# Optimization experiments

Hardware: AMD Instinct MI355X
Metric: run time of the kernel (lower is better)

Reference implementation:

```python
import jax, jax.numpy as jnp
import numpy as np

N_NODES = 100000
N_EDGES = 3200000
IN_CH = 256


def setup_inputs() -> dict:
    key = jax.random.key(0)
    k1, k2, k3 = jax.random.split(key, 3)
    x = jax.random.normal(k1, (N_NODES, IN_CH), dtype=jnp.float32)
    edge_index = jax.random.randint(k2, (2, N_EDGES), 0, N_NODES, dtype=jnp.int64)
    # GCNConv linear: weight [in_channels, 1] (applied as x @ W), bias [1]
    W = jax.random.normal(k3, (IN_CH, 1), dtype=jnp.float32) * (1.0 / np.sqrt(IN_CH))
    b = jnp.zeros((1,), dtype=jnp.float32)
    return {"x": x, "edge_index": edge_index, "W": W, "b": b}


def reference(x, edge_index, W, b):
    # PyG GCNConv(in, 1): h = x @ W; add self-loops; symmetric norm; scatter-add to target; + bias
    N = x.shape[0]
    self_loops = jnp.broadcast_to(jnp.arange(N, dtype=edge_index.dtype)[None, :], (2, N))
    ei = jnp.concatenate([edge_index, self_loops], axis=1)  # [2, E+N]
    src, dst = ei[0], ei[1]

    # degree computed at target (col) with unit edge weights, incl. self-loops
    deg = jax.ops.segment_sum(jnp.ones(ei.shape[1], dtype=x.dtype), dst, num_segments=N)
    deg_inv_sqrt = jnp.where(deg > 0, jax.lax.rsqrt(deg), 0.0)
    norm = deg_inv_sqrt[src] * deg_inv_sqrt[dst]  # [E+N]

    h = x @ W  # [N, 1] — project first (out_channels < in_channels)
    msg = norm[:, None] * h[src]  # [E+N, 1]
    out = jax.ops.segment_sum(msg, dst, num_segments=N)  # [N, 1]
    return out + b
```

## Files before the change

kernel.cpp:

```cpp
#include <hip/hip_runtime.h>

#define GCN_N 100000
#define GCN_E 3200000
#define GCN_C 256

#define BSHIFT 8
#define NBUCK 391
#define BCAP 9216
#define NBP 512
#define NB4 1024
#define CHUNK (GCN_E / NB4)
#define TB 512
#define PERTHR ((CHUNK + TB - 1) / TB)

__global__ void __launch_bounds__(TB) k_proj_hist(const float* __restrict__ x,
                                                  const float* __restrict__ W,
                                                  float* __restrict__ h,
                                                  const int* __restrict__ dst,
                                                  int* __restrict__ cnts) {
    __shared__ int hist[NBUCK];
    const int tid = threadIdx.x;

    if (blockIdx.x < NBP) {
        const int lane   = tid & 63;
        const int wave   = (blockIdx.x * TB + tid) >> 6;
        const int nwaves = NBP * (TB / 64);
        const float4 wf = *reinterpret_cast<const float4*>(W + lane * 4);
        for (int i = wave * 4; i < GCN_N; i += nwaves * 4) {
            const float4 a0 = *reinterpret_cast<const float4*>(x + (size_t)(i + 0) * GCN_C + lane * 4);
            const float4 a1 = *reinterpret_cast<const float4*>(x + (size_t)(i + 1) * GCN_C + lane * 4);
            const float4 a2 = *reinterpret_cast<const float4*>(x + (size_t)(i + 2) * GCN_C + lane * 4);
            const float4 a3 = *reinterpret_cast<const float4*>(x + (size_t)(i + 3) * GCN_C + lane * 4);
            float s0 = a0.x * wf.x + a0.y * wf.y + a0.z * wf.z + a0.w * wf.w;
            float s1 = a1.x * wf.x + a1.y * wf.y + a1.z * wf.z + a1.w * wf.w;
            float s2 = a2.x * wf.x + a2.y * wf.y + a2.z * wf.z + a2.w * wf.w;
            float s3 = a3.x * wf.x + a3.y * wf.y + a3.z * wf.z + a3.w * wf.w;
            #pragma unroll
            for (int off = 32; off > 0; off >>= 1) {
                s0 += __shfl_down(s0, off, 64);
                s1 += __shfl_down(s1, off, 64);
                s2 += __shfl_down(s2, off, 64);
                s3 += __shfl_down(s3, off, 64);
            }
            if (lane == 0) {
                h[i + 0] = s0; h[i + 1] = s1; h[i + 2] = s2; h[i + 3] = s3;
            }
        }
        return;
    }

    const int blk = blockIdx.x - NBP;
    for (int b = tid; b < NBUCK; b += TB) hist[b] = 0;
    __syncthreads();
    const int c0 = blk * CHUNK;
    for (int k = tid; k < CHUNK; k += TB)
        atomicAdd(&hist[dst[c0 + k] >> BSHIFT], 1);
    __syncthreads();
    for (int b = tid; b < NBUCK; b += TB)
        cnts[(size_t)blk * NBUCK + b] = hist[b];
}

__global__ void __launch_bounds__(1024) k_scan(int* __restrict__ cb, int* __restrict__ fill) {
    __shared__ int wsum[16], woff[16];
    const int b = blockIdx.x, tid = threadIdx.x;
    const int lane = tid & 63, w = tid >> 6;
    const int v = cb[(size_t)tid * NBUCK + b];
    int incl = v;
    #pragma unroll
    for (int d = 1; d < 64; d <<= 1) {
        const int t = __shfl_up(incl, d, 64);
        if (lane >= d) incl += t;
    }
    if (lane == 63) wsum[w] = incl;
    __syncthreads();
    if (tid == 0) {
        int s = 0;
        #pragma unroll
        for (int k = 0; k < 16; ++k) { woff[k] = s; s += wsum[k]; }
    }
    __syncthreads();
    const int excl = incl - v + woff[w];
    cb[(size_t)tid * NBUCK + b] = b * BCAP + excl;
    if (tid == 1023) fill[b] = min(excl + v, BCAP);
}

__global__ void __launch_bounds__(TB) k_place(const int* __restrict__ src,
                                              const int* __restrict__ dst,
                                              const int* __restrict__ bases,
                                              int* __restrict__ bpack) {
    __shared__ int hist[NBUCK];
    __shared__ int lscan[NBUCK];
    __shared__ int base_s[NBUCK];
    __shared__ int wsum[8], woff[8];
    __shared__ int spack[CHUNK];
    __shared__ int sdest[CHUNK];
    const int tid = threadIdx.x, blk = blockIdx.x;

    for (int b = tid; b < NBUCK; b += TB) {
        hist[b]   = 0;
        base_s[b] = bases[(size_t)blk * NBUCK + b];
    }
    __syncthreads();

    const int c0 = blk * CHUNK;
    int my_off[PERTHR];
    #pragma unroll
    for (int j = 0; j < PERTHR; ++j) {
        const int k = tid + j * TB;
        if (k < CHUNK)
            my_off[j] = atomicAdd(&hist[dst[c0 + k] >> BSHIFT], 1);
    }
    __syncthreads();

    {
        int v = (tid < NBUCK) ? hist[tid] : 0;
        const int lane = tid & 63, w = tid >> 6;
        int incl = v;
        #pragma unroll
        for (int d = 1; d < 64; d <<= 1) {
            const int t = __shfl_up(incl, d, 64);
            if (lane >= d) incl += t;
        }
        if (lane == 63) wsum[w] = incl;
        __syncthreads();
        if (tid == 0) {
            int s = 0;
            #pragma unroll
            for (int k = 0; k < 8; ++k) { woff[k] = s; s += wsum[k]; }
        }
        __syncthreads();
        if (tid < NBUCK) lscan[tid] = incl - v + woff[w];
    }
    __syncthreads();

    #pragma unroll
    for (int j = 0; j < PERTHR; ++j) {
        const int k = tid + j * TB;
        if (k < CHUNK) {
            const int d = dst[c0 + k];
            const int s = src[c0 + k];
            const int b = d >> BSHIFT;
            const int off  = my_off[j];
            const int slot = lscan[b] + off;
            const int gpos = base_s[b] + off;
            spack[slot] = (s << BSHIFT) | (d & 255);
            sdest[slot] = (gpos < (b + 1) * BCAP) ? gpos : -1;
        }
    }
    __syncthreads();

    for (int i = tid; i < CHUNK; i += TB) {
        const int dpos = sdest[i];
        if (dpos >= 0) bpack[dpos] = spack[i];
    }
}

__global__ void __launch_bounds__(1024) k_deg_norm(const int* __restrict__ bpack,
                                                   const int* __restrict__ fill,
                                                   const float* __restrict__ h,
                                                   float* __restrict__ dis,
                                                   float* __restrict__ g) {
    __shared__ int cnt[256];
    const int p = blockIdx.x, tid = threadIdx.x;
    if (tid < 256) cnt[tid] = 0;
    __syncthreads();
    const int s0 = p * BCAP, s1 = s0 + fill[p];
    for (int i = s0 + tid; i < s1; i += 1024)
        atomicAdd(&cnt[bpack[i] & 255], 1);
    __syncthreads();
    if (tid < 256) {
        const int node = (p << BSHIFT) + tid;
        if (node < GCN_N) {
            const float r = rsqrtf(1.0f + (float)cnt[tid]);
            dis[node] = r;
            g[node]   = r * h[node];
        }
    }
}

__global__ void __launch_bounds__(1024) k_scatter_bin(const int* __restrict__ bpack,
                                                      const int* __restrict__ fill,
                                                      const float* __restrict__ g,
                                                      const float* __restrict__ dis,
                                                      const float* __restrict__ bias,
                                                      float* __restrict__ out) {
    __shared__ float acc[256];
    const int p = blockIdx.x, tid = threadIdx.x;
    if (tid < 256) acc[tid] = 0.0f;
    __syncthreads();
    const int s0 = p * BCAP, s1 = s0 + fill[p];
    for (int i = s0 + tid; i < s1; i += 1024) {
        const int pk = bpack[i];
        atomicAdd(&acc[pk & 255], g[pk >> BSHIFT]);
    }
    __syncthreads();
    if (tid < 256) {
        const int node = (p << BSHIFT) + tid;
        if (node < GCN_N)
            out[node] = bias[0] + dis[node] * (acc[tid] + g[node]);
    }
}


__global__ void k_zero(float* __restrict__ a, int n) {
    int i = blockIdx.x * blockDim.x + threadIdx.x;
    const int stride = gridDim.x * blockDim.x;
    for (; i < n; i += stride) a[i] = 0.0f;
}
__global__ void k_proj_sep(const float* __restrict__ x, const float* __restrict__ W,
                           float* __restrict__ h, int n) {
    const int lane   = threadIdx.x & 63;
    const int wave   = (blockIdx.x * blockDim.x + threadIdx.x) >> 6;
    const int nwaves = (gridDim.x * blockDim.x) >> 6;
    const float4 wf = *reinterpret_cast<const float4*>(W + lane * 4);
    for (int i = wave; i < n; i += nwaves) {
        const float4 xv = *reinterpret_cast<const float4*>(x + (size_t)i * GCN_C + lane * 4);
        float s = xv.x * wf.x + xv.y * wf.y + xv.z * wf.z + xv.w * wf.w;
        #pragma unroll
        for (int off = 32; off > 0; off >>= 1)
            s += __shfl_down(s, off, 64);
        if (lane == 0) h[i] = s;
    }
}
__global__ void k_degree_flat(const int* __restrict__ dst, float* __restrict__ deg, int e) {
    int i = blockIdx.x * blockDim.x + threadIdx.x;
    const int stride = gridDim.x * blockDim.x;
    for (; i < e; i += stride) atomicAdd(&deg[dst[i]], 1.0f);
}
__global__ void k_norm_flat(const float* __restrict__ h, float* __restrict__ deg_dis,
                            float* __restrict__ out, const float* __restrict__ bias, int n) {
    const int i = blockIdx.x * blockDim.x + threadIdx.x;
    if (i < n) {
        const float r = rsqrtf(deg_dis[i] + 1.0f);
        deg_dis[i] = r;
        out[i] = bias[0] + r * r * h[i];
    }
}
__global__ void k_scatter_flat(const int* __restrict__ src, const int* __restrict__ dst,
                               const float* __restrict__ h, const float* __restrict__ dis,
                               float* __restrict__ out, int e) {
    int i = blockIdx.x * blockDim.x + threadIdx.x;
    const int stride = gridDim.x * blockDim.x;
    for (; i < e; i += stride) {
        const int s = src[i], d = dst[i];
        atomicAdd(&out[d], dis[s] * dis[d] * h[s]);
    }
}

extern "C" void kernel_launch(void* const* d_in, const int* in_sizes, int n_in,
                              void* d_out, int out_size, void* d_ws, size_t ws_size,
                              hipStream_t stream) {
    const float* x  = (const float*)d_in[0];
    const int*   ei = (const int*)d_in[1];
    const float* W  = (const float*)d_in[2];
    const float* b  = (const float*)d_in[3];
    float* out = (float*)d_out;

    const int* src = ei;
    const int* dst = ei + GCN_E;

    const size_t need = ((size_t)3 * GCN_N + NBUCK
                         + (size_t)NB4 * NBUCK
                         + (size_t)NBUCK * BCAP) * 4;
    if (ws_size >= need) {
        float* h    = (float*)d_ws;
        float* dis  = h + GCN_N;
        float* g    = dis + GCN_N;
        int*   fill = (int*)(g + GCN_N);
        int*   cb   = fill + NBUCK;
        int*   bpack = cb + (size_t)NB4 * NBUCK;

        k_proj_hist<<<NBP + NB4, TB, 0, stream>>>(x, W, h, dst, cb);
        k_scan<<<NBUCK, 1024, 0, stream>>>(cb, fill);
        k_place<<<NB4, TB, 0, stream>>>(src, dst, cb, bpack);
        k_deg_norm<<<NBUCK, 1024, 0, stream>>>(bpack, fill, h, dis, g);
        k_scatter_bin<<<NBUCK, 1024, 0, stream>>>(bpack, fill, g, dis, b, out);
    } else {
        float* h   = (float*)d_ws;
        float* deg = h + GCN_N;
        k_zero<<<512, 256, 0, stream>>>(deg, GCN_N);
        k_proj_sep<<<2048, 256, 0, stream>>>(x, W, h, GCN_N);
        k_degree_flat<<<2048, 256, 0, stream>>>(dst, deg, GCN_E);
        k_norm_flat<<<(GCN_N + 255) / 256, 256, 0, stream>>>(h, deg, out, b, GCN_N);
        k_scatter_flat<<<2048, 256, 0, stream>>>(src, dst, h, deg, out, GCN_E);
    }
}
```

Baseline: 73.14 us.

## Fuse GCN pipeline into single cooperative kernel with grid syncs

Replaces the five-kernel bucketed GCN pipeline with one cooperative kernel of 512 blocks. Grid-wide syncs separate the projection and histogram, scan, placement, degree and scatter phases. Per-block state such as edge tags, local scan and the bucket contents stays in shared memory across phases, so edges are not re-read from global memory. Placement uses a binary search over the local scan instead of a separate destination array. This removes kernel launch gaps and redundant traffic, at the cost of four grid barriers, large LDS use that limits occupancy, and reliance on cooperative launch support.

Measured after the change: 73.33 us. About the same (+0.3%).

```diff
diff --git a/kernel.cpp b/kernel.cpp
--- a/kernel.cpp
+++ b/kernel.cpp
@@ -1,17 +1,190 @@
 #include <hip/hip_runtime.h>
+#include <hip/hip_cooperative_groups.h>
+
+namespace cg = cooperative_groups;
 
 #define GCN_N 100000
 #define GCN_E 3200000
 #define GCN_C 256
-
 #define BSHIFT 8
 #define NBUCK 391
 #define BCAP 9216
+
+#define NBLK 512
+#define TBM 1024
+#define CHUNKM (GCN_E / NBLK)
+#define PERTHRM ((CHUNKM + TBM - 1) / TBM)
+
 #define NBP 512
 #define NB4 1024
 #define CHUNK (GCN_E / NB4)
 #define TB 512
 #define PERTHR ((CHUNK + TB - 1) / TB)
+
+__global__ void __launch_bounds__(TBM, 8) k_mega(
+    const float* __restrict__ x, const float* __restrict__ W,
+    const int* __restrict__ src, const int* __restrict__ dst,
+    const float* __restrict__ bias,
+    float* __restrict__ h, float* __restrict__ dis, float* __restrict__ g,
+    int* __restrict__ cnts,
+    int* __restrict__ bases,
+    int* __restrict__ fill,
+    int* __restrict__ bpack,
+    float* __restrict__ out)
+{
+    __shared__ int   spool[12500];
+    __shared__ int   hist[NBUCK];
+    __shared__ int   lscan[NBUCK];
+    __shared__ int   base_s[NBUCK];
+    __shared__ int   wsum[16], woff[16];
+    __shared__ float accf[256];
+
+    const int tid = threadIdx.x;
+    const int blk = blockIdx.x;
+    int* spack = spool;
+    int* tmp   = spool + CHUNKM;
+    cg::grid_group grid = cg::this_grid();
+
+    for (int p = tid; p < NBUCK; p += TBM) hist[p] = 0;
+    __syncthreads();
+    const int c0 = blk * CHUNKM;
+    #pragma unroll
+    for (int j = 0; j < PERTHRM; ++j) {
+        const int k = tid + j * TBM;
+        if (k < CHUNKM) {
+            const int d   = dst[c0 + k];
+            const int b   = d >> BSHIFT;
+            const int off = atomicAdd(&hist[b], 1);
+            tmp[k] = (b << 21) | ((d & 255) << 13) | off;
+        }
+    }
+    __syncthreads();
+
+    if (tid < NBUCK) cnts[(size_t)tid * NBLK + blk] = hist[tid];
+    {
+        const int lane = tid & 63, w = tid >> 6;
+        const int v = (tid < NBUCK) ? hist[tid] : 0;
+        int incl = v;
+        #pragma unroll
+        for (int d2 = 1; d2 < 64; d2 <<= 1) {
+            const int t = __shfl_up(incl, d2, 64);
+            if (lane >= d2) incl += t;
+        }
+        if (lane == 63 && w < 7) wsum[w] = incl;
+        __syncthreads();
+        if (tid == 0) { int s = 0; for (int k2 = 0; k2 < 7; ++k2) { woff[k2] = s; s += wsum[k2]; } }
+        __syncthreads();
+        if (tid < NBUCK) lscan[tid] = incl - v + woff[w];
+    }
+
+    {
+        const int lane = tid & 63;
+        const int wave = (blk * TBM + tid) >> 6;
+        const int step = NBLK * (TBM / 64) * 4;
+        const float4 wf = *reinterpret_cast<const float4*>(W + lane * 4);
+        for (int i = wave * 4; i < GCN_N; i += step) {
+            const float4 a0 = *reinterpret_cast<const float4*>(x + (size_t)(i + 0) * GCN_C + lane * 4);
+            const float4 a1 = *reinterpret_cast<const float4*>(x + (size_t)(i + 1) * GCN_C + lane * 4);
+            const float4 a2 = *reinterpret_cast<const float4*>(x + (size_t)(i + 2) * GCN_C + lane * 4);
+            const float4 a3 = *reinterpret_cast<const float4*>(x + (size_t)(i + 3) * GCN_C + lane * 4);
+            float s0 = a0.x * wf.x + a0.y * wf.y + a0.z * wf.z + a0.w * wf.w;
+            float s1 = a1.x * wf.x + a1.y * wf.y + a1.z * wf.z + a1.w * wf.w;
+            float s2 = a2.x * wf.x + a2.y * wf.y + a2.z * wf.z + a2.w * wf.w;
+            float s3 = a3.x * wf.x + a3.y * wf.y + a3.z * wf.z + a3.w * wf.w;
+            #pragma unroll
+            for (int off = 32; off > 0; off >>= 1) {
+                s0 += __shfl_down(s0, off, 64);
+                s1 += __shfl_down(s1, off, 64);
+                s2 += __shfl_down(s2, off, 64);
+                s3 += __shfl_down(s3, off, 64);
+            }
+            if (lane == 0) { h[i] = s0; h[i + 1] = s1; h[i + 2] = s2; h[i + 3] = s3; }
+        }
+    }
+    grid.sync();
+
+    if (blk < NBUCK) {
+        const int v = (tid < NBLK) ? cnts[(size_t)blk * NBLK + tid] : 0;
+        const int lane = tid & 63, w = tid >> 6;
+        int incl = v;
+        #pragma unroll
+        for (int d2 = 1; d2 < 64; d2 <<= 1) {
+            const int t = __shfl_up(incl, d2, 64);
+            if (lane >= d2) incl += t;
+        }
+        if (lane == 63 && w < 8) wsum[w] = incl;
+        __syncthreads();
+        if (tid == 0) { int s = 0; for (int k2 = 0; k2 < 8; ++k2) { woff[k2] = s; s += wsum[k2]; } }
+        __syncthreads();
+        if (tid < NBLK) {
+            const int excl = incl - v + woff[w];
+            bases[(size_t)blk * NBLK + tid] = blk * BCAP + excl;
+            if (tid == NBLK - 1) fill[blk] = min(excl + v, BCAP);
+        }
+    }
+    grid.sync();
+
+    for (int p = tid; p < NBUCK; p += TBM) base_s[p] = bases[(size_t)p * NBLK + blk];
+    __syncthreads();
+    #pragma unroll
+    for (int j = 0; j < PERTHRM; ++j) {
+        const int k = tid + j * TBM;
+        if (k < CHUNKM) {
+            const int t   = tmp[k];
+            const int b   = t >> 21;
+            const int d8  = (t >> 13) & 255;
+            const int off = t & 8191;
+            const int s   = src[c0 + k];
+            spack[lscan[b] + off] = (s << BSHIFT) | d8;
+        }
+    }
+    __syncthreads();
+    for (int i = tid; i < CHUNKM; i += TBM) {
+        int lo = 0, hi = NBUCK;
+        while (hi - lo > 1) { const int mid = (lo + hi) >> 1; if (lscan[mid] <= i) lo = mid; else hi = mid; }
+        const int gpos = base_s[lo] + (i - lscan[lo]);
+        if (gpos < (lo + 1) * BCAP) bpack[gpos] = spack[i];
+    }
+    grid.sync();
+
+    int fillp = 0;
+    if (blk < NBUCK) {
+        fillp = fill[blk];
+        int* cnt = hist;
+        if (tid < 256) cnt[tid] = 0;
+        __syncthreads();
+        const size_t s0 = (size_t)blk * BCAP;
+        for (int i = tid; i < fillp; i += TBM) spool[i] = bpack[s0 + i];
+        __syncthreads();
+        for (int i = tid; i < fillp; i += TBM) atomicAdd(&cnt[spool[i] & 255], 1);
+        __syncthreads();
+        if (tid < 256) {
+            const int node = (blk << BSHIFT) + tid;
+            if (node < GCN_N) {
+                const float r = rsqrtf(1.0f + (float)cnt[tid]);
+                dis[node] = r;
+                g[node]   = r * h[node];
+            }
+        }
+    }
+    grid.sync();
+
+    if (blk < NBUCK) {
+        if (tid < 256) accf[tid] = 0.0f;
+        __syncthreads();
+        for (int i = tid; i < fillp; i += TBM) {
+            const int pk = spool[i];
+            atomicAdd(&accf[pk & 255], g[pk >> BSHIFT]);
+        }
+        __syncthreads();
+        if (tid < 256) {
+            const int node = (blk << BSHIFT) + tid;
+            if (node < GCN_N)
+                out[node] = bias[0] + dis[node] * (accf[tid] + g[node]);
+        }
+    }
+}
+
 
 __global__ void __launch_bounds__(TB) k_proj_hist(const float* __restrict__ x,
                                                   const float* __restrict__ W,
@@ -20,7 +193,6 @@
                                                   int* __restrict__ cnts) {
     __shared__ int hist[NBUCK];
     const int tid = threadIdx.x;
-
     if (blockIdx.x < NBP) {
         const int lane   = tid & 63;
         const int wave   = (blockIdx.x * TB + tid) >> 6;
@@ -42,13 +214,10 @@
                 s2 += __shfl_down(s2, off, 64);
                 s3 += __shfl_down(s3, off, 64);
             }
-            if (lane == 0) {
-                h[i + 0] = s0; h[i + 1] = s1; h[i + 2] = s2; h[i + 3] = s3;
-            }
+            if (lane == 0) { h[i] = s0; h[i + 1] = s1; h[i + 2] = s2; h[i + 3] = s3; }
         }
         return;
     }
-
     const int blk = blockIdx.x - NBP;
     for (int b = tid; b < NBUCK; b += TB) hist[b] = 0;
     __syncthreads();
@@ -73,11 +242,7 @@
     }
     if (lane == 63) wsum[w] = incl;
     __syncthreads();
-    if (tid == 0) {
-        int s = 0;
-        #pragma unroll
-        for (int k = 0; k < 16; ++k) { woff[k] = s; s += wsum[k]; }
-    }
+    if (tid == 0) { int s = 0; for (int k = 0; k < 16; ++k) { woff[k] = s; s += wsum[k]; } }
     __syncthreads();
     const int excl = incl - v + woff[w];
     cb[(size_t)tid * NBUCK + b] = b * BCAP + excl;
@@ -95,13 +260,11 @@
     __shared__ int spack[CHUNK];
     __shared__ int sdest[CHUNK];
     const int tid = threadIdx.x, blk = blockIdx.x;
-
     for (int b = tid; b < NBUCK; b += TB) {
         hist[b]   = 0;
         base_s[b] = bases[(size_t)blk * NBUCK + b];
     }
     __syncthreads();
-
     const int c0 = blk * CHUNK;
     int my_off[PERTHR];
     #pragma unroll
@@ -111,9 +274,8 @@
             my_off[j] = atomicAdd(&hist[dst[c0 + k] >> BSHIFT], 1);
     }
     __syncthreads();
-
     {
-        int v = (tid < NBUCK) ? hist[tid] : 0;
+        const int v = (tid < NBUCK) ? hist[tid] : 0;
         const int lane = tid & 63, w = tid >> 6;
         int incl = v;
         #pragma unroll
@@ -123,16 +285,11 @@
         }
         if (lane == 63) wsum[w] = incl;
         __syncthreads();
-        if (tid == 0) {
-            int s = 0;
-            #pragma unroll
-            for (int k = 0; k < 8; ++k) { woff[k] = s; s += wsum[k]; }
-        }
+        if (tid == 0) { int s = 0; for (int k = 0; k < 8; ++k) { woff[k] = s; s += wsum[k]; } }
         __syncthreads();
         if (tid < NBUCK) lscan[tid] = incl - v + woff[w];
     }
     __syncthreads();
-
     #pragma unroll
     for (int j = 0; j < PERTHR; ++j) {
         const int k = tid + j * TB;
@@ -148,7 +305,6 @@
         }
     }
     __syncthreads();
-
     for (int i = tid; i < CHUNK; i += TB) {
         const int dpos = sdest[i];
         if (dpos >= 0) bpack[dpos] = spack[i];
@@ -201,52 +357,6 @@
     }
 }
 
-
-__global__ void k_zero(float* __restrict__ a, int n) {
-    int i = blockIdx.x * blockDim.x + threadIdx.x;
-    const int stride = gridDim.x * blockDim.x;
-    for (; i < n; i += stride) a[i] = 0.0f;
-}
-__global__ void k_proj_sep(const float* __restrict__ x, const float* __restrict__ W,
-                           float* __restrict__ h, int n) {
-    const int lane   = threadIdx.x & 63;
-    const int wave   = (blockIdx.x * blockDim.x + threadIdx.x) >> 6;
-    const int nwaves = (gridDim.x * blockDim.x) >> 6;
-    const float4 wf = *reinterpret_cast<const float4*>(W + lane * 4);
-    for (int i = wave; i < n; i += nwaves) {
-        const float4 xv = *reinterpret_cast<const float4*>(x + (size_t)i * GCN_C + lane * 4);
-        float s = xv.x * wf.x + xv.y * wf.y + xv.z * wf.z + xv.w * wf.w;
-        #pragma unroll
-        for (int off = 32; off > 0; off >>= 1)
-            s += __shfl_down(s, off, 64);
-        if (lane == 0) h[i] = s;
-    }
-}
-__global__ void k_degree_flat(const int* __restrict__ dst, float* __restrict__ deg, int e) {
-    int i = blockIdx.x * blockDim.x + threadIdx.x;
-    const int stride = gridDim.x * blockDim.x;
-    for (; i < e; i += stride) atomicAdd(&deg[dst[i]], 1.0f);
-}
-__global__ void k_norm_flat(const float* __restrict__ h, float* __restrict__ deg_dis,
-                            float* __restrict__ out, const float* __restrict__ bias, int n) {
-    const int i = blockIdx.x * blockDim.x + threadIdx.x;
-    if (i < n) {
-        const float r = rsqrtf(deg_dis[i] + 1.0f);
-        deg_dis[i] = r;
-        out[i] = bias[0] + r * r * h[i];
-    }
-}
-__global__ void k_scatter_flat(const int* __restrict__ src, const int* __restrict__ dst,
-                               const float* __restrict__ h, const float* __restrict__ dis,
-                               float* __restrict__ out, int e) {
-    int i = blockIdx.x * blockDim.x + threadIdx.x;
-    const int stride = gridDim.x * blockDim.x;
-    for (; i < e; i += stride) {
-        const int s = src[i], d = dst[i];
-        atomicAdd(&out[d], dis[s] * dis[d] * h[s]);
-    }
-}
-
 extern "C" void kernel_launch(void* const* d_in, const int* in_sizes, int n_in,
                               void* d_out, int out_size, void* d_ws, size_t ws_size,
                               hipStream_t stream) {
@@ -255,33 +365,39 @@
     const float* W  = (const float*)d_in[2];
     const float* b  = (const float*)d_in[3];
     float* out = (float*)d_out;
-
     const int* src = ei;
     const int* dst = ei + GCN_E;
 
-    const size_t need = ((size_t)3 * GCN_N + NBUCK
-                         + (size_t)NB4 * NBUCK
+    float* h    = (float*)d_ws;
+    float* dis  = h + GCN_N;
+    float* g    = dis + GCN_N;
+    int*   fill = (int*)(g + GCN_N);
+    int*   cnts = fill + NBUCK;
+    int*   bases = cnts + (size_t)NBLK * NBUCK;
+    int*   bpack = bases + (size_t)NBLK * NBUCK;
+    const size_t need = ((size_t)3 * GCN_N + NBUCK + 2ull * NBLK * NBUCK
                          + (size_t)NBUCK * BCAP) * 4;
-    if (ws_size >= need) {
-        float* h    = (float*)d_ws;
-        float* dis  = h + GCN_N;
-        float* g    = dis + GCN_N;
-        int*   fill = (int*)(g + GCN_N);
-        int*   cb   = fill + NBUCK;
-        int*   bpack = cb + (size_t)NB4 * NBUCK;
-
+
+    int dev = 0; (void)hipGetDevice(&dev);
+    int coopAttr = 0, numCU = 0, maxBpc = 0;
+    (void)hipDeviceGetAttribute(&coopAttr, hipDeviceAttributeCooperativeLaunch, dev);
+    (void)hipDeviceGetAttribute(&numCU, hipDeviceAttributeMultiprocessorCount, dev);
+    hipError_t qe = hipOccupancyMaxActiveBlocksPerMultiprocessor(&maxBpc, k_mega, TBM, 0);
+    const bool coop = (ws_size >= need) && coopAttr && (qe == hipSuccess) &&
+                      ((long long)maxBpc * numCU >= NBLK);
+
+    if (coop) {
+        void* args[] = {(void*)&x, (void*)&W, (void*)&src, (void*)&dst, (void*)&b,
+                        (void*)&h, (void*)&dis, (void*)&g,
+                        (void*)&cnts, (void*)&bases, (void*)&fill, (void*)&bpack,
+                        (void*)&out};
+        (void)hipLaunchCooperativeKernel(k_mega, dim3(NBLK), dim3(TBM), args, 0, stream);
+    } else if (ws_size >= need) {
+        int* cb = cnts;
         k_proj_hist<<<NBP + NB4, TB, 0, stream>>>(x, W, h, dst, cb);
         k_scan<<<NBUCK, 1024, 0, stream>>>(cb, fill);
         k_place<<<NB4, TB, 0, stream>>>(src, dst, cb, bpack);
         k_deg_norm<<<NBUCK, 1024, 0, stream>>>(bpack, fill, h, dis, g);
         k_scatter_bin<<<NBUCK, 1024, 0, stream>>>(bpack, fill, g, dis, b, out);
-    } else {
-        float* h   = (float*)d_ws;
-        float* deg = h + GCN_N;
-        k_zero<<<512, 256, 0, stream>>>(deg, GCN_N);
-        k_proj_sep<<<2048, 256, 0, stream>>>(x, W, h, GCN_N);
-        k_degree_flat<<<2048, 256, 0, stream>>>(dst, deg, GCN_E);
-        k_norm_flat<<<(GCN_N + 255) / 256, 256, 0, stream>>>(h, deg, out, b, GCN_N);
-        k_scatter_flat<<<2048, 256, 0, stream>>>(src, dst, h, deg, out, GCN_E);
-    }
-}
+    }
+}
```
